# Performance work log

Measured on AMD Instinct MI355X. Metric: run time of the kernel, lower is better.

## Reference

```python
import jax, jax.numpy as jnp
import numpy as np

N_NODES = 20000
N_EDGES = 320000
IN_CH = 512
HEADS = 4
OUT_CH = 128
NEG_SLOPE = 0.2  # PyG GATConv default leaky_relu slope


def setup_inputs() -> dict:
    key = jax.random.key(0)
    k1, k2, k3, k4, k5 = jax.random.split(key, 5)
    x = jax.random.normal(k1, (N_NODES, IN_CH), dtype=jnp.float32)
    edge_index = jax.random.randint(k2, (2, N_EDGES), 0, N_NODES, dtype=jnp.int64)
    # Learned parameters (glorot-ish scaling)
    W = jax.random.normal(k3, (IN_CH, HEADS * OUT_CH), dtype=jnp.float32) * np.float32(1.0 / np.sqrt(IN_CH))
    att_src = jax.random.normal(k4, (HEADS, OUT_CH), dtype=jnp.float32) * np.float32(0.1)
    att_dst = jax.random.normal(k5, (HEADS, OUT_CH), dtype=jnp.float32) * np.float32(0.1)
    bias = jnp.zeros((OUT_CH,), dtype=jnp.float32)
    return {"x": x, "W": W, "att_src": att_src, "att_dst": att_dst, "bias": bias, "edge_index": edge_index}


def reference(x, W, att_src, att_dst, bias, edge_index):
    N = x.shape[0]
    H, C = att_src.shape
    # add self-loops (PyG GATConv default add_self_loops=True)
    loop = jnp.arange(N, dtype=edge_index.dtype)
    ei = jnp.concatenate([edge_index, jnp.stack([loop, loop])], axis=1)
    src, dst = ei[0], ei[1]
    # linear projection: [N, H, C]
    xl = (x @ W).reshape(N, H, C)
    # per-node attention halves: [N, H]
    a_s = jnp.einsum('nhc,hc->nh', xl, att_src)
    a_d = jnp.einsum('nhc,hc->nh', xl, att_dst)
    # per-edge logits + segment softmax over incoming edges (grouped by dst)
    alpha = jax.nn.leaky_relu(a_s[src] + a_d[dst], negative_slope=NEG_SLOPE)  # [E, H]
    amax = jax.ops.segment_max(alpha, dst, num_segments=N)  # every node has a self-loop -> no empty segments
    ae = jnp.exp(alpha - amax[dst])
    denom = jax.ops.segment_sum(ae, dst, num_segments=N)
    alpha = ae / (denom[dst] + 1e-16)
    # weighted scatter-add of source features: [N, H, C]
    out = jax.ops.segment_sum(alpha[:, :, None] * xl[src], dst, num_segments=N)
    # concat=False -> mean over heads, then bias [C]
    out = out.mean(axis=1) + bias
    return jax.nn.elu(out)
```

## Files before the change

kernel.cpp:

```cpp
#include <hip/hip_runtime.h>
#include <math.h>

#define N_NODES 20000
#define N_PAD 20096
#define N_EDGES 320000
#define IN_CH 512
#define HEADS 4
#define OUT_CH 128
#define HC 512
#define NEG_SLOPE 0.2f

#define CVX_BLOCKS 5024
#define CVW_BLOCKS 64
#define CNT_BLOCKS 1250
#define SCT_BLOCKS 1250
#define ATT_BLOCKS 5000

typedef __attribute__((ext_vector_type(8))) short short8;
typedef __attribute__((ext_vector_type(4))) float float4v;

__device__ __forceinline__ int detect_is64(const int* __restrict__ ei32) {
    int is64 = 1;
    #pragma unroll
    for (int i = 0; i < 32; i++) is64 &= (ei32[2 * i + 1] == 0);
    return is64;
}

__device__ __forceinline__ int edge_at(const void* ei, int is64, long long idx) {
    return is64 ? (int)((const long long*)ei)[idx] : ((const int*)ei)[idx];
}

__device__ __forceinline__ unsigned short f2bf(float f) {
    union { float f; unsigned u; } v; v.f = f;
    unsigned r = v.u + 0x7fffu + ((v.u >> 16) & 1u);
    return (unsigned short)(r >> 16);
}

__device__ __forceinline__ void bf8_decode(uint4 r, float* f) {
    f[0] = __uint_as_float(r.x << 16); f[1] = __uint_as_float(r.x & 0xffff0000u);
    f[2] = __uint_as_float(r.y << 16); f[3] = __uint_as_float(r.y & 0xffff0000u);
    f[4] = __uint_as_float(r.z << 16); f[5] = __uint_as_float(r.z & 0xffff0000u);
    f[6] = __uint_as_float(r.w << 16); f[7] = __uint_as_float(r.w & 0xffff0000u);
}

__device__ __forceinline__ float leaky(float t) { return t > 0.f ? t : NEG_SLOPE * t; }

__global__ __launch_bounds__(256) void fusedA_kernel(const float* __restrict__ x,
                                                     const float* __restrict__ W,
                                                     unsigned short* __restrict__ xb,
                                                     unsigned short* __restrict__ Wt,
                                                     const void* __restrict__ ei,
                                                     int* __restrict__ counts) {
    __shared__ float tile[64][65];
    int b = blockIdx.x;
    if (b < CVX_BLOCKS) {
        size_t i = ((size_t)b * 256 + threadIdx.x) * 8;
        unsigned short o[8];
        if (i < (size_t)N_NODES * IN_CH) {
            float4 f0 = *(const float4*)&x[i];
            float4 f1 = *(const float4*)&x[i + 4];
            o[0] = f2bf(f0.x); o[1] = f2bf(f0.y); o[2] = f2bf(f0.z); o[3] = f2bf(f0.w);
            o[4] = f2bf(f1.x); o[5] = f2bf(f1.y); o[6] = f2bf(f1.z); o[7] = f2bf(f1.w);
        } else {
            for (int k = 0; k < 8; k++) o[k] = 0;
        }
        *(short8*)&xb[i] = *(short8*)o;
    } else if (b < CVX_BLOCKS + CVW_BLOCKS) {
        int idx = b - CVX_BLOCKS;
        int k0 = (idx & 7) * 64, n0 = (idx >> 3) * 64;
        int t = threadIdx.x, r = t >> 6, c = t & 63;
        for (int rr = r; rr < 64; rr += 4)
            tile[rr][c] = W[(size_t)(k0 + rr) * HC + n0 + c];
        __syncthreads();
        for (int rr = r; rr < 64; rr += 4)
            Wt[(size_t)(n0 + rr) * IN_CH + k0 + c] = f2bf(tile[c][rr]);
    } else {
        int is64 = detect_is64((const int*)ei);
        int e = (b - CVX_BLOCKS - CVW_BLOCKS) * 256 + threadIdx.x;
        if (e < N_EDGES) {
            int dst = edge_at(ei, is64, (long long)N_EDGES + e);
            atomicAdd(&counts[dst], 1);
        }
    }
}

__global__ __launch_bounds__(256) void gemm_kernel(const unsigned short* __restrict__ A,
                                                   const unsigned short* __restrict__ Bt,
                                                   unsigned short* __restrict__ Cb) {
    __shared__ __align__(16) unsigned short As[128 * 32];
    __shared__ __align__(16) unsigned short Bs[128 * 32];
    const int bm = blockIdx.y * 128;
    const int bn = blockIdx.x * 128;
    const int t = threadIdx.x;
    const int wv = t >> 6, lane = t & 63;
    const int wm = wv & 1, wn = wv >> 1;
    const int lm = lane & 15, lk = lane >> 4;

    float4v acc[4][4];
    #pragma unroll
    for (int i = 0; i < 4; i++)
        #pragma unroll
        for (int j = 0; j < 4; j++) acc[i][j] = (float4v){0.f, 0.f, 0.f, 0.f};

    const int srow = t >> 2;
    const int skof = (t & 3) * 8;

    for (int k0 = 0; k0 < IN_CH; k0 += 32) {
        __syncthreads();
        #pragma unroll
        for (int q = 0; q < 2; q++) {
            const unsigned short* gA = A + (size_t)(bm + q * 64 + srow) * IN_CH + k0 + skof;
            const unsigned short* gB = Bt + (size_t)(bn + q * 64 + srow) * IN_CH + k0 + skof;
            __builtin_amdgcn_global_load_lds((const __attribute__((address_space(1))) void*)gA,
                                             (__attribute__((address_space(3))) void*)&As[q * 2048 + t * 8], 16, 0, 0);
            __builtin_amdgcn_global_load_lds((const __attribute__((address_space(1))) void*)gB,
                                             (__attribute__((address_space(3))) void*)&Bs[q * 2048 + t * 8], 16, 0, 0);
        }
        __syncthreads();

        short8 af[4], bf[4];
        #pragma unroll
        for (int i = 0; i < 4; i++)
            af[i] = *(const short8*)&As[(wm * 64 + i * 16 + lm) * 32 + lk * 8];
        #pragma unroll
        for (int j = 0; j < 4; j++)
            bf[j] = *(const short8*)&Bs[(wn * 64 + j * 16 + lm) * 32 + lk * 8];
        #pragma unroll
        for (int i = 0; i < 4; i++)
            #pragma unroll
            for (int j = 0; j < 4; j++)
                acc[i][j] = __builtin_amdgcn_mfma_f32_16x16x32_bf16(af[i], bf[j], acc[i][j], 0, 0, 0);
    }

    #pragma unroll
    for (int i = 0; i < 4; i++) {
        #pragma unroll
        for (int r = 0; r < 4; r++) {
            int row = bm + wm * 64 + i * 16 + lk * 4 + r;
            if (row < N_NODES) {
                #pragma unroll
                for (int j = 0; j < 4; j++) {
                    int col = bn + wn * 64 + j * 16 + lm;
                    Cb[(size_t)row * HC + col] = f2bf(acc[i][j][r]);
                }
            }
        }
    }
}

__global__ __launch_bounds__(1024) void scan_kernel(const int* __restrict__ counts,
                                                    int* __restrict__ offsets) {
    const int CHUNK = 20;
    int tid = threadIdx.x;
    int base = tid * CHUNK;
    int c[CHUNK];
    #pragma unroll
    for (int k = 0; k < CHUNK; k++) {
        int i = base + k;
        c[k] = (i < N_NODES) ? counts[i] : 0;
    }
    int pre[CHUNK];
    int sum = 0;
    #pragma unroll
    for (int k = 0; k < CHUNK; k++) { pre[k] = sum; sum += c[k]; }

    int lane = tid & 63, wv = tid >> 6;
    int s = sum;
    #pragma unroll
    for (int off = 1; off < 64; off <<= 1) {
        int u = __shfl_up(s, off, 64);
        if (lane >= off) s += u;
    }
    __shared__ int wsum[16];
    if (lane == 63) wsum[wv] = s;
    __syncthreads();
    if (tid < 16) {
        int u = wsum[tid];
        #pragma unroll
        for (int off = 1; off < 16; off <<= 1) {
            int w = __shfl_up(u, off, 64);
            if (tid >= off) u += w;
        }
        wsum[tid] = u;
    }
    __syncthreads();
    int wbase = (wv == 0) ? 0 : wsum[wv - 1];
    int excl = wbase + s - sum;
    #pragma unroll
    for (int k = 0; k < CHUNK; k++) {
        int i = base + k;
        if (i < N_NODES) offsets[i] = excl + pre[k];
    }
    if (tid == 1023) offsets[N_NODES] = wbase + s;
}

__global__ __launch_bounds__(256) void fusedB_kernel(const void* __restrict__ ei,
                                                     const int* __restrict__ offsets,
                                                     int* __restrict__ cursor,
                                                     int* __restrict__ sorted_src,
                                                     const unsigned short* __restrict__ xlb,
                                                     const float* __restrict__ att_s,
                                                     const float* __restrict__ att_d,
                                                     float* __restrict__ a_s,
                                                     float* __restrict__ a_d) {
    int b = blockIdx.x;
    if (b < SCT_BLOCKS) {
        int is64 = detect_is64((const int*)ei);
        int e = b * 256 + threadIdx.x;
        if (e < N_EDGES) {
            int dst = edge_at(ei, is64, (long long)N_EDGES + e);
            int src = edge_at(ei, is64, e);
            int pos = offsets[dst] + atomicAdd(&cursor[dst], 1);
            sorted_src[pos] = src;
        }
    } else {
        int node = (b - SCT_BLOCKS) * 4 + (threadIdx.x >> 6);
        if (node >= N_NODES) return;
        int lane = threadIdx.x & 63;
        int hd = lane >> 4;
        uint4 r = *(const uint4*)&xlb[(size_t)node * HC + lane * 8];
        float f[8];
        bf8_decode(r, f);
        float4 s0 = *(const float4*)&att_s[lane * 8];
        float4 s1 = *(const float4*)&att_s[lane * 8 + 4];
        float4 d0 = *(const float4*)&att_d[lane * 8];
        float4 d1 = *(const float4*)&att_d[lane * 8 + 4];
        float s = f[0]*s0.x + f[1]*s0.y + f[2]*s0.z + f[3]*s0.w
                + f[4]*s1.x + f[5]*s1.y + f[6]*s1.z + f[7]*s1.w;
        float d = f[0]*d0.x + f[1]*d0.y + f[2]*d0.z + f[3]*d0.w
                + f[4]*d1.x + f[5]*d1.y + f[6]*d1.z + f[7]*d1.w;
        #pragma unroll
        for (int off = 1; off < 16; off <<= 1) {
            s += __shfl_xor(s, off, 64);
            d += __shfl_xor(d, off, 64);
        }
        if ((lane & 15) == 0) {
            a_s[node * 4 + hd] = s;
            a_d[node * 4 + hd] = d;
        }
    }
}

__global__ __launch_bounds__(256) void gather_kernel(const unsigned short* __restrict__ xlb,
                                                     const float* __restrict__ a_s,
                                                     const float* __restrict__ a_d,
                                                     const int* __restrict__ offsets,
                                                     const int* __restrict__ sorted_src,
                                                     const float* __restrict__ bias,
                                                     float* __restrict__ out) {
    int node = blockIdx.x * 4 + (threadIdx.x >> 6);
    if (node >= N_NODES) return;
    int lane = threadIdx.x & 63;
    int hd = lane >> 4;
    int beg = offsets[node], end = offsets[node + 1];

    const unsigned short* xrow = xlb + lane * 8;
    float adh = a_d[node * 4 + hd];
    float acc[8];
    float denom;
    {
        float w = __expf(leaky(a_s[node * 4 + hd] + adh));
        denom = w;
        uint4 r = *(const uint4*)(xrow + (size_t)node * HC);
        float f[8];
        bf8_decode(r, f);
        #pragma unroll
        for (int k = 0; k < 8; k++) acc[k] = w * f[k];
    }
    int p = beg;
    for (; p + 4 <= end; p += 4) {
        int s0 = sorted_src[p];
        int s1 = sorted_src[p + 1];
        int s2 = sorted_src[p + 2];
        int s3 = sorted_src[p + 3];
        uint4 r0 = *(const uint4*)(xrow + (size_t)s0 * HC);
        uint4 r1 = *(const uint4*)(xrow + (size_t)s1 * HC);
        uint4 r2 = *(const uint4*)(xrow + (size_t)s2 * HC);
        uint4 r3 = *(const uint4*)(xrow + (size_t)s3 * HC);
        float w0 = __expf(leaky(a_s[s0 * 4 + hd] + adh));
        float w1 = __expf(leaky(a_s[s1 * 4 + hd] + adh));
        float w2 = __expf(leaky(a_s[s2 * 4 + hd] + adh));
        float w3 = __expf(leaky(a_s[s3 * 4 + hd] + adh));
        denom += (w0 + w1) + (w2 + w3);
        float f0[8], f1[8], f2[8], f3[8];
        bf8_decode(r0, f0);
        bf8_decode(r1, f1);
        bf8_decode(r2, f2);
        bf8_decode(r3, f3);
        #pragma unroll
        for (int k = 0; k < 8; k++)
            acc[k] += (w0 * f0[k] + w1 * f1[k]) + (w2 * f2[k] + w3 * f3[k]);
    }
    for (; p < end; p++) {
        int s0 = sorted_src[p];
        uint4 r0 = *(const uint4*)(xrow + (size_t)s0 * HC);
        float w0 = __expf(leaky(a_s[s0 * 4 + hd] + adh));
        denom += w0;
        float f0[8];
        bf8_decode(r0, f0);
        #pragma unroll
        for (int k = 0; k < 8; k++) acc[k] += w0 * f0[k];
    }

    float rd = 0.25f / (denom + 1e-16f);
    float v[8];
    #pragma unroll
    for (int k = 0; k < 8; k++) {
        float t = acc[k] * rd;
        t += __shfl_xor(t, 16, 64);
        t += __shfl_xor(t, 32, 64);
        v[k] = t;
    }
    if (hd == 0) {
        float4 b0 = *(const float4*)&bias[lane * 8];
        float4 b1 = *(const float4*)&bias[lane * 8 + 4];
        float o[8];
        o[0] = v[0] + b0.x; o[1] = v[1] + b0.y; o[2] = v[2] + b0.z; o[3] = v[3] + b0.w;
        o[4] = v[4] + b1.x; o[5] = v[5] + b1.y; o[6] = v[6] + b1.z; o[7] = v[7] + b1.w;
        #pragma unroll
        for (int k = 0; k < 8; k++) o[k] = o[k] > 0.f ? o[k] : expm1f(o[k]);
        *(float4*)&out[(size_t)node * OUT_CH + lane * 8]     = make_float4(o[0], o[1], o[2], o[3]);
        *(float4*)&out[(size_t)node * OUT_CH + lane * 8 + 4] = make_float4(o[4], o[5], o[6], o[7]);
    }
}

extern "C" void kernel_launch(void* const* d_in, const int* in_sizes, int n_in,
                              void* d_out, int out_size, void* d_ws, size_t ws_size,
                              hipStream_t stream) {
    const float* x       = (const float*)d_in[0];
    const float* W       = (const float*)d_in[1];
    const float* att_src = (const float*)d_in[2];
    const float* att_dst = (const float*)d_in[3];
    const float* bias    = (const float*)d_in[4];
    const void*  ei      = d_in[5];
    float* out = (float*)d_out;

    char* ws = (char*)d_ws;
    size_t off = 0;
    unsigned short* xlb = (unsigned short*)(ws + off); off += (size_t)N_PAD * HC * sizeof(unsigned short);
    float* a_s     = (float*)(ws + off); off += (size_t)N_NODES * HEADS * sizeof(float);
    float* a_d     = (float*)(ws + off); off += (size_t)N_NODES * HEADS * sizeof(float);
    int* counts    = (int*)(ws + off);   off += (size_t)N_NODES * sizeof(int);
    int* cursor    = (int*)(ws + off);   off += (size_t)N_NODES * sizeof(int);
    int* offsets   = (int*)(ws + off);   off += (size_t)(N_NODES + 1) * sizeof(int);
    off = (off + 15) & ~(size_t)15;
    int* sorted_src = (int*)(ws + off);  off += (size_t)N_EDGES * sizeof(int);
    off = (off + 15) & ~(size_t)15;
    unsigned short* xb = (unsigned short*)(ws + off); off += (size_t)N_PAD * IN_CH * sizeof(unsigned short);
    unsigned short* Wt = (unsigned short*)(ws + off); off += (size_t)IN_CH * HC * sizeof(unsigned short);

    hipMemsetAsync(counts, 0, 2u * N_NODES * sizeof(int), stream);
    fusedA_kernel<<<CVX_BLOCKS + CVW_BLOCKS + CNT_BLOCKS, 256, 0, stream>>>(x, W, xb, Wt, ei, counts);
    gemm_kernel<<<dim3(HC / 128, N_PAD / 128), 256, 0, stream>>>(xb, Wt, xlb);
    scan_kernel<<<1, 1024, 0, stream>>>(counts, offsets);
    fusedB_kernel<<<SCT_BLOCKS + ATT_BLOCKS, 256, 0, stream>>>(ei, offsets, cursor, sorted_src,
                                                               xlb, att_src, att_dst, a_s, a_d);
    gather_kernel<<<(N_NODES + 3) / 4, 256, 0, stream>>>(xlb, a_s, a_d, offsets, sorted_src, bias, out);
}
```

Measured before the change: 216.9 us.

## Precompute per-edge exp weights in scatter and split gather across two waves

Fuses the scan and per-node attention-logit computation into one launch. The CSR scatter kernel now also computes the exponentiated leaky-relu edge weights for all four heads and stores them in sorted order. The gather kernel reads these weights instead of doing random a_s lookups and exps, and splits each node's edge list across two wavefronts that combine partial sums through shared memory. This adds a 5 MB edge-weight buffer write and read, plus a block barrier, in exchange for fewer dependent random loads and more parallelism per node.

```diff
diff --git a/kernel.cpp b/kernel.cpp
--- a/kernel.cpp
+++ b/kernel.cpp
@@ -13,8 +13,7 @@
 #define CVX_BLOCKS 5024
 #define CVW_BLOCKS 64
 #define CNT_BLOCKS 1250
-#define SCT_BLOCKS 1250
-#define ATT_BLOCKS 5000
+#define ATT_BLOCKS 1250
 
 typedef __attribute__((ext_vector_type(8))) short short8;
 typedef __attribute__((ext_vector_type(4))) float float4v;
@@ -44,6 +43,12 @@
 }
 
 __device__ __forceinline__ float leaky(float t) { return t > 0.f ? t : NEG_SLOPE * t; }
+
+__device__ __forceinline__ float sel_head(float4 w, int hd) {
+    float lo = (hd & 1) ? w.y : w.x;
+    float hi = (hd & 1) ? w.w : w.z;
+    return (hd & 2) ? hi : lo;
+}
 
 __global__ __launch_bounds__(256) void fusedA_kernel(const float* __restrict__ x,
                                                      const float* __restrict__ W,
@@ -148,73 +153,59 @@
     }
 }
 
-__global__ __launch_bounds__(1024) void scan_kernel(const int* __restrict__ counts,
-                                                    int* __restrict__ offsets) {
-    const int CHUNK = 20;
-    int tid = threadIdx.x;
-    int base = tid * CHUNK;
-    int c[CHUNK];
-    #pragma unroll
-    for (int k = 0; k < CHUNK; k++) {
-        int i = base + k;
-        c[k] = (i < N_NODES) ? counts[i] : 0;
-    }
-    int pre[CHUNK];
-    int sum = 0;
-    #pragma unroll
-    for (int k = 0; k < CHUNK; k++) { pre[k] = sum; sum += c[k]; }
-
-    int lane = tid & 63, wv = tid >> 6;
-    int s = sum;
-    #pragma unroll
-    for (int off = 1; off < 64; off <<= 1) {
-        int u = __shfl_up(s, off, 64);
-        if (lane >= off) s += u;
-    }
-    __shared__ int wsum[16];
-    if (lane == 63) wsum[wv] = s;
-    __syncthreads();
-    if (tid < 16) {
-        int u = wsum[tid];
-        #pragma unroll
-        for (int off = 1; off < 16; off <<= 1) {
-            int w = __shfl_up(u, off, 64);
-            if (tid >= off) u += w;
-        }
-        wsum[tid] = u;
-    }
-    __syncthreads();
-    int wbase = (wv == 0) ? 0 : wsum[wv - 1];
-    int excl = wbase + s - sum;
-    #pragma unroll
-    for (int k = 0; k < CHUNK; k++) {
-        int i = base + k;
-        if (i < N_NODES) offsets[i] = excl + pre[k];
-    }
-    if (tid == 1023) offsets[N_NODES] = wbase + s;
-}
-
-__global__ __launch_bounds__(256) void fusedB_kernel(const void* __restrict__ ei,
-                                                     const int* __restrict__ offsets,
-                                                     int* __restrict__ cursor,
-                                                     int* __restrict__ sorted_src,
-                                                     const unsigned short* __restrict__ xlb,
-                                                     const float* __restrict__ att_s,
-                                                     const float* __restrict__ att_d,
-                                                     float* __restrict__ a_s,
-                                                     float* __restrict__ a_d) {
+__global__ __launch_bounds__(1024) void scanattn_kernel(const int* __restrict__ counts,
+                                                        int* __restrict__ offsets,
+                                                        const unsigned short* __restrict__ xlb,
+                                                        const float* __restrict__ att_s,
+                                                        const float* __restrict__ att_d,
+                                                        float* __restrict__ a_s,
+                                                        float* __restrict__ a_d) {
     int b = blockIdx.x;
-    if (b < SCT_BLOCKS) {
-        int is64 = detect_is64((const int*)ei);
-        int e = b * 256 + threadIdx.x;
-        if (e < N_EDGES) {
-            int dst = edge_at(ei, is64, (long long)N_EDGES + e);
-            int src = edge_at(ei, is64, e);
-            int pos = offsets[dst] + atomicAdd(&cursor[dst], 1);
-            sorted_src[pos] = src;
-        }
+    if (b == 0) {
+        const int CHUNK = 20;
+        int tid = threadIdx.x;
+        int base = tid * CHUNK;
+        int c[CHUNK];
+        #pragma unroll
+        for (int k = 0; k < CHUNK; k++) {
+            int i = base + k;
+            c[k] = (i < N_NODES) ? counts[i] : 0;
+        }
+        int pre[CHUNK];
+        int sum = 0;
+        #pragma unroll
+        for (int k = 0; k < CHUNK; k++) { pre[k] = sum; sum += c[k]; }
+
+        int lane = tid & 63, wvv = tid >> 6;
+        int s = sum;
+        #pragma unroll
+        for (int off = 1; off < 64; off <<= 1) {
+            int u = __shfl_up(s, off, 64);
+            if (lane >= off) s += u;
+        }
+        __shared__ int wsum[16];
+        if (lane == 63) wsum[wvv] = s;
+        __syncthreads();
+        if (tid < 16) {
+            int u = wsum[tid];
+            #pragma unroll
+            for (int off = 1; off < 16; off <<= 1) {
+                int w = __shfl_up(u, off, 64);
+                if (tid >= off) u += w;
+            }
+            wsum[tid] = u;
+        }
+        __syncthreads();
+        int wbase = (wvv == 0) ? 0 : wsum[wvv - 1];
+        int excl = wbase + s - sum;
+        #pragma unroll
+        for (int k = 0; k < CHUNK; k++) {
+            int i = base + k;
+            if (i < N_NODES) offsets[i] = excl + pre[k];
+        }
+        if (tid == 1023) offsets[N_NODES] = wbase + s;
     } else {
-        int node = (b - SCT_BLOCKS) * 4 + (threadIdx.x >> 6);
+        int node = (b - 1) * 16 + (threadIdx.x >> 6);
         if (node >= N_NODES) return;
         int lane = threadIdx.x & 63;
         int hd = lane >> 4;
@@ -241,25 +232,61 @@
     }
 }
 
+__global__ __launch_bounds__(256) void scatterw_kernel(const void* __restrict__ ei,
+                                                       const int* __restrict__ offsets,
+                                                       int* __restrict__ cursor,
+                                                       int* __restrict__ sorted_src,
+                                                       const float* __restrict__ a_s,
+                                                       const float* __restrict__ a_d,
+                                                       float* __restrict__ edge_w) {
+    int is64 = detect_is64((const int*)ei);
+    int e = blockIdx.x * 256 + threadIdx.x;
+    if (e < N_EDGES) {
+        int dst = edge_at(ei, is64, (long long)N_EDGES + e);
+        int src = edge_at(ei, is64, e);
+        int pos = offsets[dst] + atomicAdd(&cursor[dst], 1);
+        sorted_src[pos] = src;
+        float4 as4 = *(const float4*)&a_s[src * 4];
+        float4 ad4 = *(const float4*)&a_d[dst * 4];
+        float4 w;
+        w.x = __expf(leaky(as4.x + ad4.x));
+        w.y = __expf(leaky(as4.y + ad4.y));
+        w.z = __expf(leaky(as4.z + ad4.z));
+        w.w = __expf(leaky(as4.w + ad4.w));
+        *(float4*)&edge_w[(size_t)pos * 4] = w;
+    }
+}
+
 __global__ __launch_bounds__(256) void gather_kernel(const unsigned short* __restrict__ xlb,
                                                      const float* __restrict__ a_s,
                                                      const float* __restrict__ a_d,
                                                      const int* __restrict__ offsets,
                                                      const int* __restrict__ sorted_src,
+                                                     const float* __restrict__ edge_w,
                                                      const float* __restrict__ bias,
                                                      float* __restrict__ out) {
-    int node = blockIdx.x * 4 + (threadIdx.x >> 6);
-    if (node >= N_NODES) return;
+    __shared__ float cl[2][64][9];
+    int wv = threadIdx.x >> 6;
+    int nib = wv >> 1;
+    int sub = wv & 1;
+    int node = blockIdx.x * 2 + nib;
     int lane = threadIdx.x & 63;
     int hd = lane >> 4;
     int beg = offsets[node], end = offsets[node + 1];
 
     const unsigned short* xrow = xlb + lane * 8;
-    float adh = a_d[node * 4 + hd];
-    float acc[8];
-    float denom;
-    {
-        float w = __expf(leaky(a_s[node * 4 + hd] + adh));
+    float acc[8] = {0, 0, 0, 0, 0, 0, 0, 0};
+    float denom = 0.f;
+
+    if (sub == 0) {
+        float4 as4 = *(const float4*)&a_s[node * 4];
+        float4 ad4 = *(const float4*)&a_d[node * 4];
+        float4 ws;
+        ws.x = __expf(leaky(as4.x + ad4.x));
+        ws.y = __expf(leaky(as4.y + ad4.y));
+        ws.z = __expf(leaky(as4.z + ad4.z));
+        ws.w = __expf(leaky(as4.w + ad4.w));
+        float w = sel_head(ws, hd);
         denom = w;
         uint4 r = *(const uint4*)(xrow + (size_t)node * HC);
         float f[8];
@@ -267,60 +294,79 @@
         #pragma unroll
         for (int k = 0; k < 8; k++) acc[k] = w * f[k];
     }
-    int p = beg;
-    for (; p + 4 <= end; p += 4) {
-        int s0 = sorted_src[p];
-        int s1 = sorted_src[p + 1];
-        int s2 = sorted_src[p + 2];
-        int s3 = sorted_src[p + 3];
-        uint4 r0 = *(const uint4*)(xrow + (size_t)s0 * HC);
-        uint4 r1 = *(const uint4*)(xrow + (size_t)s1 * HC);
-        uint4 r2 = *(const uint4*)(xrow + (size_t)s2 * HC);
-        uint4 r3 = *(const uint4*)(xrow + (size_t)s3 * HC);
-        float w0 = __expf(leaky(a_s[s0 * 4 + hd] + adh));
-        float w1 = __expf(leaky(a_s[s1 * 4 + hd] + adh));
-        float w2 = __expf(leaky(a_s[s2 * 4 + hd] + adh));
-        float w3 = __expf(leaky(a_s[s3 * 4 + hd] + adh));
-        denom += (w0 + w1) + (w2 + w3);
-        float f0[8], f1[8], f2[8], f3[8];
-        bf8_decode(r0, f0);
-        bf8_decode(r1, f1);
-        bf8_decode(r2, f2);
-        bf8_decode(r3, f3);
-        #pragma unroll
-        for (int k = 0; k < 8; k++)
-            acc[k] += (w0 * f0[k] + w1 * f1[k]) + (w2 * f2[k] + w3 * f3[k]);
-    }
-    for (; p < end; p++) {
-        int s0 = sorted_src[p];
-        uint4 r0 = *(const uint4*)(xrow + (size_t)s0 * HC);
-        float w0 = __expf(leaky(a_s[s0 * 4 + hd] + adh));
-        denom += w0;
-        float f0[8];
-        bf8_decode(r0, f0);
-        #pragma unroll
-        for (int k = 0; k < 8; k++) acc[k] += w0 * f0[k];
-    }
-
-    float rd = 0.25f / (denom + 1e-16f);
-    float v[8];
-    #pragma unroll
-    for (int k = 0; k < 8; k++) {
-        float t = acc[k] * rd;
-        t += __shfl_xor(t, 16, 64);
-        t += __shfl_xor(t, 32, 64);
-        v[k] = t;
-    }
-    if (hd == 0) {
-        float4 b0 = *(const float4*)&bias[lane * 8];
-        float4 b1 = *(const float4*)&bias[lane * 8 + 4];
-        float o[8];
-        o[0] = v[0] + b0.x; o[1] = v[1] + b0.y; o[2] = v[2] + b0.z; o[3] = v[3] + b0.w;
-        o[4] = v[4] + b1.x; o[5] = v[5] + b1.y; o[6] = v[6] + b1.z; o[7] = v[7] + b1.w;
-        #pragma unroll
-        for (int k = 0; k < 8; k++) o[k] = o[k] > 0.f ? o[k] : expm1f(o[k]);
-        *(float4*)&out[(size_t)node * OUT_CH + lane * 8]     = make_float4(o[0], o[1], o[2], o[3]);
-        *(float4*)&out[(size_t)node * OUT_CH + lane * 8 + 4] = make_float4(o[4], o[5], o[6], o[7]);
+
+    for (int c0 = beg + sub * 4; c0 < end; c0 += 8) {
+        int n = end - c0;
+        if (n >= 4) {
+            int s0 = sorted_src[c0];
+            int s1 = sorted_src[c0 + 1];
+            int s2 = sorted_src[c0 + 2];
+            int s3 = sorted_src[c0 + 3];
+            uint4 r0 = *(const uint4*)(xrow + (size_t)s0 * HC);
+            uint4 r1 = *(const uint4*)(xrow + (size_t)s1 * HC);
+            uint4 r2 = *(const uint4*)(xrow + (size_t)s2 * HC);
+            uint4 r3 = *(const uint4*)(xrow + (size_t)s3 * HC);
+            float4 wa = *(const float4*)&edge_w[(size_t)c0 * 4];
+            float4 wb = *(const float4*)&edge_w[(size_t)(c0 + 1) * 4];
+            float4 wc = *(const float4*)&edge_w[(size_t)(c0 + 2) * 4];
+            float4 wd = *(const float4*)&edge_w[(size_t)(c0 + 3) * 4];
+            float w0 = sel_head(wa, hd), w1 = sel_head(wb, hd);
+            float w2 = sel_head(wc, hd), w3 = sel_head(wd, hd);
+            denom += (w0 + w1) + (w2 + w3);
+            float f0[8], f1[8], f2[8], f3[8];
+            bf8_decode(r0, f0);
+            bf8_decode(r1, f1);
+            bf8_decode(r2, f2);
+            bf8_decode(r3, f3);
+            #pragma unroll
+            for (int k = 0; k < 8; k++)
+                acc[k] += (w0 * f0[k] + w1 * f1[k]) + (w2 * f2[k] + w3 * f3[k]);
+        } else {
+            for (int j = 0; j < n; j++) {
+                int s0 = sorted_src[c0 + j];
+                uint4 r0 = *(const uint4*)(xrow + (size_t)s0 * HC);
+                float4 wa = *(const float4*)&edge_w[(size_t)(c0 + j) * 4];
+                float w0 = sel_head(wa, hd);
+                denom += w0;
+                float f0[8];
+                bf8_decode(r0, f0);
+                #pragma unroll
+                for (int k = 0; k < 8; k++) acc[k] += w0 * f0[k];
+            }
+        }
+    }
+
+    if (sub == 1) {
+        #pragma unroll
+        for (int k = 0; k < 8; k++) cl[nib][lane][k] = acc[k];
+        cl[nib][lane][8] = denom;
+    }
+    __syncthreads();
+    if (sub == 0) {
+        #pragma unroll
+        for (int k = 0; k < 8; k++) acc[k] += cl[nib][lane][k];
+        denom += cl[nib][lane][8];
+
+        float rd = 0.25f / (denom + 1e-16f);
+        float v[8];
+        #pragma unroll
+        for (int k = 0; k < 8; k++) {
+            float t = acc[k] * rd;
+            t += __shfl_xor(t, 16, 64);
+            t += __shfl_xor(t, 32, 64);
+            v[k] = t;
+        }
+        if (hd == 0) {
+            float4 b0 = *(const float4*)&bias[lane * 8];
+            float4 b1 = *(const float4*)&bias[lane * 8 + 4];
+            float o[8];
+            o[0] = v[0] + b0.x; o[1] = v[1] + b0.y; o[2] = v[2] + b0.z; o[3] = v[3] + b0.w;
+            o[4] = v[4] + b1.x; o[5] = v[5] + b1.y; o[6] = v[6] + b1.z; o[7] = v[7] + b1.w;
+            #pragma unroll
+            for (int k = 0; k < 8; k++) o[k] = o[k] > 0.f ? o[k] : expm1f(o[k]);
+            *(float4*)&out[(size_t)node * OUT_CH + lane * 8]     = make_float4(o[0], o[1], o[2], o[3]);
+            *(float4*)&out[(size_t)node * OUT_CH + lane * 8 + 4] = make_float4(o[4], o[5], o[6], o[7]);
+        }
     }
 }
 
@@ -346,14 +392,14 @@
     off = (off + 15) & ~(size_t)15;
     int* sorted_src = (int*)(ws + off);  off += (size_t)N_EDGES * sizeof(int);
     off = (off + 15) & ~(size_t)15;
+    float* edge_w  = (float*)(ws + off); off += (size_t)N_EDGES * HEADS * sizeof(float);
     unsigned short* xb = (unsigned short*)(ws + off); off += (size_t)N_PAD * IN_CH * sizeof(unsigned short);
     unsigned short* Wt = (unsigned short*)(ws + off); off += (size_t)IN_CH * HC * sizeof(unsigned short);
 
     hipMemsetAsync(counts, 0, 2u * N_NODES * sizeof(int), stream);
     fusedA_kernel<<<CVX_BLOCKS + CVW_BLOCKS + CNT_BLOCKS, 256, 0, stream>>>(x, W, xb, Wt, ei, counts);
     gemm_kernel<<<dim3(HC / 128, N_PAD / 128), 256, 0, stream>>>(xb, Wt, xlb);
-    scan_kernel<<<1, 1024, 0, stream>>>(counts, offsets);
-    fusedB_kernel<<<SCT_BLOCKS + ATT_BLOCKS, 256, 0, stream>>>(ei, offsets, cursor, sorted_src,
-                                                               xlb, att_src, att_dst, a_s, a_d);
-    gather_kernel<<<(N_NODES + 3) / 4, 256, 0, stream>>>(xlb, a_s, a_d, offsets, sorted_src, bias, out);
-}
+    scanattn_kernel<<<1 + ATT_BLOCKS, 1024, 0, stream>>>(counts, offsets, xlb, att_src, att_dst, a_s, a_d);
+    scatterw_kernel<<<(N_EDGES + 255) / 256, 256, 0, stream>>>(ei, offsets, cursor, sorted_src, a_s, a_d, edge_w);
+    gather_kernel<<<N_NODES / 2, 256, 0, stream>>>(xlb, a_s, a_d, offsets, sorted_src, edge_w, bias, out);
+}
```

Result: no change. 215.3 us (-0.7%).
